# Kernel optimization log

Measured on AMD Instinct MI355X. Metric: run time of the kernel, lower is better.

## Reference

```python
import jax, jax.numpy as jnp
import numpy as np
from jax import lax


def setup_inputs() -> dict:
    key = jax.random.key(0)
    k0, k1, k2, k3 = jax.random.split(key, 4)
    B, Ct, Ht, Wt = 8, 16, 16, 16
    Cm, Hm, Wm = 16, 128, 128
    Cout, K = 64, 3
    template = jax.random.normal(k0, (B, Ct, Ht, Wt), jnp.float32)
    tomatch = jax.random.normal(k1, (B, Cm, Hm, Wm), jnp.float32)
    fan_in = Ct * Cm * K * K
    bound = 1.0 / np.sqrt(fan_in)
    W = jax.random.uniform(k2, (Cout, Ct * Cm, K, K), jnp.float32, -bound, bound)
    b = jax.random.uniform(k3, (Cout,), jnp.float32, -bound, bound)
    return {"template": template, "tomatch": tomatch, "W": W, "b": b}


def _dense_corr(template, tomatch):
    # template: [B, Ct, Ht, Wt], tomatch: [B, Cm, Hm, Wm]
    B, Ct, Ht, Wt = template.shape
    _, Cm, Hm, Wm = tomatch.shape
    # ReplicationPad2d((0, Wt-1, 0, Ht-1)) -> edge pad right/bottom only
    padded = jnp.pad(tomatch, ((0, 0), (0, 0), (0, Ht - 1), (0, Wt - 1)), mode="edge")

    def per_example(tm_pad, tp):
        # tm_pad: [Cm, Hm+Ht-1, Wm+Wt-1] -> treat Cm as batch with 1 channel
        # tp: [Ct, Ht, Wt] -> Ct single-channel filters
        out = lax.conv_general_dilated(
            tm_pad[:, None, :, :],  # [Cm, 1, Hp, Wp] NCHW
            tp[:, None, :, :],      # [Ct, 1, Ht, Wt] OIHW
            window_strides=(1, 1),
            padding="VALID",
        )  # [Cm, Ct, Hm, Wm] (torch conv2d = cross-correlation, same as lax)
        return out.reshape(Cm * Ct, Hm, Wm)  # channel = cm*Ct + ct, matches torch .view

    return jax.vmap(per_example)(padded, template)  # [B, Cm*Ct, Hm, Wm]


def reference(template, tomatch, W, b):
    corr = _dense_corr(template, tomatch)  # [B, Cm*Ct, Hm, Wm]
    out = lax.conv_general_dilated(corr, W, (1, 1), "SAME")  # 3x3 'same' merge conv
    return out + b[None, :, None, None]
```

## Files before the change

kernel.cpp:

```cpp
#include <hip/hip_runtime.h>
#include <hip/hip_bf16.h>


typedef __attribute__((ext_vector_type(4))) float  f32x4;
typedef __attribute__((ext_vector_type(8))) short  bf16x8;

__device__ inline unsigned int pack_bf16x2(float a, float b) {
    unsigned int ua = __builtin_bit_cast(unsigned int, a);
    unsigned int ub = __builtin_bit_cast(unsigned int, b);
    ua = (ua + 0x7fffu + ((ua >> 16) & 1u)) >> 16;
    ub = (ub + 0x7fffu + ((ub >> 16) & 1u)) >> 16;
    return ua | (ub << 16);
}
__device__ inline unsigned short cvt1(float f) {
    unsigned int u = __builtin_bit_cast(unsigned int, f);
    return (unsigned short)((u + 0x7fffu + ((u >> 16) & 1u)) >> 16);
}

__global__ __launch_bounds__(256) void corr_mfma(
    const float* __restrict__ tp, const float* __restrict__ tm,
    unsigned short* __restrict__ corrb)
{
    __shared__ __align__(16) unsigned short smA[2 * 2 * 31 * 82];

    const int t    = threadIdx.x;
    const int wave = t >> 6, lane = t & 63;
    const int n    = lane & 15, quad = lane >> 4;
    const int qh   = quad >> 1, jq = quad & 1;

    const int xh   = (int)blockIdx.x & 1;
    const int y0   = ((int)blockIdx.x >> 1) << 4;
    const int pair = (int)blockIdx.y & 7;
    const int b    = (int)blockIdx.y >> 3;
    const int xg0  = xh << 6;

    for (int cm2 = 0; cm2 < 2; ++cm2) {
        const float* src = tm + (((size_t)(b * 16 + pair * 2 + cm2)) << 14);
        for (int e = t; e < 31 * 80; e += 256) {
            int r = e / 80, c = e - r * 80;
            int gy = y0 + r;  gy = gy > 127 ? 127 : gy;
            int gx = xg0 + c; gx = gx > 127 ? 127 : gx;
            unsigned short h = cvt1(src[(gy << 7) + gx]);
            smA[((cm2 * 2 + 0) * 31 + r) * 82 + c] = h;
            if (c > 0)
                smA[((cm2 * 2 + 1) * 31 + r) * 82 + (c - 1)] = h;
        }
    }
    __syncthreads();

    bf16x8 bq[8];
    {
        const float* tpb = tp + (((size_t)(b * 16 + n)) << 8);
#pragma unroll
        for (int kc = 0; kc < 8; ++kc) {
            const float4* q = (const float4*)(tpb + (((2 * kc + qh) << 4) + (jq << 3)));
            float4 a = q[0], c4 = q[1];
            union { uint4 u; bf16x8 h; } cv;
            cv.u.x = pack_bf16x2(a.x, a.y);
            cv.u.y = pack_bf16x2(a.z, a.w);
            cv.u.z = pack_bf16x2(c4.x, c4.y);
            cv.u.w = pack_bf16x2(c4.z, c4.w);
            bq[kc] = cv.h;
        }
    }

    const unsigned* smAd = (const unsigned*)smA;
    const int PITCH = 41, PLANE = 31 * 41;

#pragma unroll 1
    for (int it = 0; it < 8; ++it) {
        const int lxa  = (wave << 4) + (it << 1);
        const int D00  = (n + qh) * PITCH + ((lxa + (jq << 3)) >> 1);

        f32x4 acc[4];
#pragma unroll
        for (int q = 0; q < 4; ++q) acc[q] = (f32x4){0.f, 0.f, 0.f, 0.f};

#pragma unroll
        for (int kc = 0; kc < 8; ++kc) {
            const int dof = D00 + kc * 82;
#pragma unroll
            for (int ch = 0; ch < 4; ++ch) {
                const int d = dof + ch * PLANE;
                union { uint4 u; bf16x8 h; } fr;
                fr.u.x = smAd[d];     fr.u.y = smAd[d + 1];
                fr.u.z = smAd[d + 2]; fr.u.w = smAd[d + 3];
                const int ai = ((ch & 1) << 1) | (ch >> 1);
                acc[ai] = __builtin_amdgcn_mfma_f32_16x16x32_bf16(
                    bq[kc], fr.h, acc[ai], 0, 0, 0);
            }
        }

        const int y = y0 + n;
#pragma unroll
        for (int ai = 0; ai < 4; ++ai) {
            const int par = ai >> 1, cm2 = ai & 1;
            const int x   = xg0 + lxa + par;
            uint2 v;
            v.x = pack_bf16x2(acc[ai][0], acc[ai][1]);
            v.y = pack_bf16x2(acc[ai][2], acc[ai][3]);
            unsigned short* dst = corrb
                + (((size_t)(b * 16384 + (y << 7) + x)) << 8)
                + (pair << 5) + (cm2 << 4) + (quad << 2);
            *(uint2*)dst = v;
        }
    }
}

__global__ __launch_bounds__(256) void wt_kernel(
    const float* __restrict__ W, unsigned short* __restrict__ Wb)
{
    int idx = (int)blockIdx.x * 256 + (int)threadIdx.x;
    int c  = idx & 255;
    int rem = idx >> 8;
    int co = rem % 64;
    int kk = rem / 64;
    Wb[idx] = cvt1(W[(size_t)co * 2304 + (size_t)c * 9 + kk]);
}

__global__ __launch_bounds__(256) void merge_mfma(
    const unsigned short* __restrict__ corrb, const unsigned short* __restrict__ Wb,
    const float* __restrict__ bias, float* __restrict__ out)
{
    __shared__ __align__(16) unsigned short sm[10 * 34 * 72];

    const int t    = threadIdx.x;
    const int wave = t >> 6, lane = t & 63;
    const int n    = lane & 15, quad = lane >> 4;
    const int x0   = (int)blockIdx.x << 5;
    const int y0   = (int)blockIdx.y << 3;
    const int b    = (int)blockIdx.z;

    f32x4 acc[4][4];
#pragma unroll
    for (int a = 0; a < 4; ++a)
#pragma unroll
        for (int q = 0; q < 4; ++q) acc[a][q] = (f32x4){0.f, 0.f, 0.f, 0.f};

    const unsigned short* cb = corrb + ((size_t)b << 22);

    uint4 v[11];

#define SLAB_LOAD(C0)                                                        \
    {                                                                        \
        _Pragma("unroll")                                                    \
        for (int k = 0; k < 11; ++k) {                                       \
            int e = t + (k << 8);                                            \
            int ci = e & 7, rem = e >> 3;                                    \
            int cc = rem % 34, r = rem / 34;                                 \
            int gy = y0 - 1 + r, gx = x0 - 1 + cc;                           \
            uint4 vv = {0u, 0u, 0u, 0u};                                     \
            if (e < 2720 && (unsigned)gy < 128u && (unsigned)gx < 128u)      \
                vv = *(const uint4*)(cb + (((size_t)((gy << 7) + gx)) << 8)  \
                                        + (C0) + (ci << 3));                 \
            v[k] = vv;                                                       \
        }                                                                    \
    }
#define SLAB_WRITE()                                                         \
    {                                                                        \
        _Pragma("unroll")                                                    \
        for (int k = 0; k < 11; ++k) {                                       \
            int e = t + (k << 8);                                            \
            int ci = e & 7, rem = e >> 3;                                    \
            int cc = rem % 34, r = rem / 34;                                 \
            if (e < 2720)                                                    \
                *(uint4*)&sm[r * 2448 + cc * 72 + (ci << 3)] = v[k];         \
        }                                                                    \
    }

    SLAB_LOAD(0)
    SLAB_WRITE()
    __syncthreads();

#pragma unroll 1
    for (int c0 = 0; c0 < 256; c0 += 64) {
        if (c0 < 192) SLAB_LOAD(c0 + 64)

        const unsigned short* wpb = Wb + (size_t)n * 256 + c0 + (quad << 3);
        bf16x8 afc[4];
        {
#pragma unroll
            for (int ct = 0; ct < 4; ++ct)
                afc[ct] = *(const bf16x8*)(wpb + (size_t)ct * 4096);
        }
#pragma unroll 1
        for (int idx = 0; idx < 18; ++idx) {
            const int nidx = idx < 17 ? idx + 1 : 17;
            const int nkk = nidx >> 1, nkc = nidx & 1;
            bf16x8 afn[4];
#pragma unroll
            for (int ct = 0; ct < 4; ++ct)
                afn[ct] = *(const bf16x8*)(wpb + (size_t)nkk * 16384
                                               + (nkc << 5) + (size_t)ct * 4096);
            const int kk = idx >> 1, kc = idx & 1;
            const int dy = kk / 3, dx = kk - 3 * dy;
#pragma unroll
            for (int nt = 0; nt < 4; ++nt) {
                const int prow = 2 * wave + (nt >> 1) + dy;
                const int pcol = ((nt & 1) << 4) + n + dx;
                bf16x8 bf = *(const bf16x8*)&sm[prow * 2448 + pcol * 72
                                                + (kc << 5) + (quad << 3)];
#pragma unroll
                for (int ct = 0; ct < 4; ++ct)
                    acc[ct][nt] = __builtin_amdgcn_mfma_f32_16x16x32_bf16(
                        afc[ct], bf, acc[ct][nt], 0, 0, 0);
            }
#pragma unroll
            for (int ct = 0; ct < 4; ++ct) afc[ct] = afn[ct];
        }

        __syncthreads();
        if (c0 < 192) SLAB_WRITE()
        __syncthreads();
    }

#pragma unroll
    for (int ct = 0; ct < 4; ++ct) {
#pragma unroll
        for (int nt = 0; nt < 4; ++nt) {
            const int y   = y0 + 2 * wave + (nt >> 1);
            const int x   = x0 + ((nt & 1) << 4) + n;
            const int co0 = (ct << 4) + (quad << 2);
            float* op = out + (((size_t)((b << 6) + co0) << 7) + y) * 128 + x;
#pragma unroll
            for (int r = 0; r < 4; ++r)
                op[(size_t)r << 14] = acc[ct][nt][r] + bias[co0 + r];
        }
    }
#undef SLAB_LOAD
#undef SLAB_WRITE
}

extern "C" void kernel_launch(void* const* d_in, const int* in_sizes, int n_in,
                              void* d_out, int out_size, void* d_ws, size_t ws_size,
                              hipStream_t stream)
{
    const float* tp   = (const float*)d_in[0];
    const float* tm   = (const float*)d_in[1];
    const float* Wt   = (const float*)d_in[2];
    const float* bias = (const float*)d_in[3];
    float* out = (float*)d_out;

    unsigned short* corrb = (unsigned short*)d_ws;
    unsigned short* Wb    = corrb + (size_t)8 * 16384 * 256;

    corr_mfma<<<dim3(16, 64), dim3(256), 0, stream>>>(tp, tm, corrb);
    wt_kernel<<<dim3(576), dim3(256), 0, stream>>>(Wt, Wb);
    merge_mfma<<<dim3(4, 16, 8), dim3(256), 0, stream>>>(corrb, Wb, bias, out);
}
```

Before: 193.6 us.

## Fuse correlation into merge conv, recomputing corr tile with halo in shared memory

Merges the correlation kernel and the 3x3 merge conv into one kernel. Each block computes the bf16 correlation for its 10x34 halo tile directly into shared memory, one group of 4 template-match channels (64 corr channels) per stage, then runs the merge MFMAs on it. This drops the large bf16 corr intermediate in global memory and its write/read traffic. In exchange it recomputes the halo correlation, serializes the corr and merge phases with barriers and no overlap, and moves to 512 threads per block.

```diff
diff --git a/kernel.cpp b/kernel.cpp
--- a/kernel.cpp
+++ b/kernel.cpp
@@ -17,36 +17,33 @@
     return (unsigned short)((u + 0x7fffu + ((u >> 16) & 1u)) >> 16);
 }
 
-__global__ __launch_bounds__(256) void corr_mfma(
+__global__ __launch_bounds__(256) void wt_kernel(
+    const float* __restrict__ W, unsigned short* __restrict__ Wb)
+{
+    int idx = (int)blockIdx.x * 256 + (int)threadIdx.x;
+    int c  = idx & 255;
+    int rem = idx >> 8;
+    int co = rem % 64;
+    int kk = rem / 64;
+    Wb[idx] = cvt1(W[(size_t)co * 2304 + (size_t)c * 9 + kk]);
+}
+
+__global__ __launch_bounds__(512, 4) void fused_mfma(
     const float* __restrict__ tp, const float* __restrict__ tm,
-    unsigned short* __restrict__ corrb)
+    const unsigned short* __restrict__ Wb, const float* __restrict__ bias,
+    float* __restrict__ out)
 {
-    __shared__ __align__(16) unsigned short smA[2 * 2 * 31 * 82];
+    __shared__ __align__(16) unsigned short smC[10 * 34 * 72];
+    __shared__ __align__(16) unsigned short smT[4 * 2 * 25 * 50];
 
     const int t    = threadIdx.x;
     const int wave = t >> 6, lane = t & 63;
     const int n    = lane & 15, quad = lane >> 4;
     const int qh   = quad >> 1, jq = quad & 1;
 
-    const int xh   = (int)blockIdx.x & 1;
-    const int y0   = ((int)blockIdx.x >> 1) << 4;
-    const int pair = (int)blockIdx.y & 7;
-    const int b    = (int)blockIdx.y >> 3;
-    const int xg0  = xh << 6;
-
-    for (int cm2 = 0; cm2 < 2; ++cm2) {
-        const float* src = tm + (((size_t)(b * 16 + pair * 2 + cm2)) << 14);
-        for (int e = t; e < 31 * 80; e += 256) {
-            int r = e / 80, c = e - r * 80;
-            int gy = y0 + r;  gy = gy > 127 ? 127 : gy;
-            int gx = xg0 + c; gx = gx > 127 ? 127 : gx;
-            unsigned short h = cvt1(src[(gy << 7) + gx]);
-            smA[((cm2 * 2 + 0) * 31 + r) * 82 + c] = h;
-            if (c > 0)
-                smA[((cm2 * 2 + 1) * 31 + r) * 82 + (c - 1)] = h;
-        }
-    }
-    __syncthreads();
+    const int x0 = (int)blockIdx.x << 5;
+    const int y0 = (int)blockIdx.y << 3;
+    const int b  = (int)blockIdx.z;
 
     bf16x8 bq[8];
     {
@@ -64,162 +61,108 @@
         }
     }
 
-    const unsigned* smAd = (const unsigned*)smA;
-    const int PITCH = 41, PLANE = 31 * 41;
-
-#pragma unroll 1
-    for (int it = 0; it < 8; ++it) {
-        const int lxa  = (wave << 4) + (it << 1);
-        const int D00  = (n + qh) * PITCH + ((lxa + (jq << 3)) >> 1);
-
-        f32x4 acc[4];
-#pragma unroll
-        for (int q = 0; q < 4; ++q) acc[q] = (f32x4){0.f, 0.f, 0.f, 0.f};
-
-#pragma unroll
-        for (int kc = 0; kc < 8; ++kc) {
-            const int dof = D00 + kc * 82;
-#pragma unroll
-            for (int ch = 0; ch < 4; ++ch) {
-                const int d = dof + ch * PLANE;
-                union { uint4 u; bf16x8 h; } fr;
-                fr.u.x = smAd[d];     fr.u.y = smAd[d + 1];
-                fr.u.z = smAd[d + 2]; fr.u.w = smAd[d + 3];
-                const int ai = ((ch & 1) << 1) | (ch >> 1);
-                acc[ai] = __builtin_amdgcn_mfma_f32_16x16x32_bf16(
-                    bq[kc], fr.h, acc[ai], 0, 0, 0);
-            }
-        }
-
-        const int y = y0 + n;
-#pragma unroll
-        for (int ai = 0; ai < 4; ++ai) {
-            const int par = ai >> 1, cm2 = ai & 1;
-            const int x   = xg0 + lxa + par;
-            uint2 v;
-            v.x = pack_bf16x2(acc[ai][0], acc[ai][1]);
-            v.y = pack_bf16x2(acc[ai][2], acc[ai][3]);
-            unsigned short* dst = corrb
-                + (((size_t)(b * 16384 + (y << 7) + x)) << 8)
-                + (pair << 5) + (cm2 << 4) + (quad << 2);
-            *(uint2*)dst = v;
-        }
-    }
-}
-
-__global__ __launch_bounds__(256) void wt_kernel(
-    const float* __restrict__ W, unsigned short* __restrict__ Wb)
-{
-    int idx = (int)blockIdx.x * 256 + (int)threadIdx.x;
-    int c  = idx & 255;
-    int rem = idx >> 8;
-    int co = rem % 64;
-    int kk = rem / 64;
-    Wb[idx] = cvt1(W[(size_t)co * 2304 + (size_t)c * 9 + kk]);
-}
-
-__global__ __launch_bounds__(256) void merge_mfma(
-    const unsigned short* __restrict__ corrb, const unsigned short* __restrict__ Wb,
-    const float* __restrict__ bias, float* __restrict__ out)
-{
-    __shared__ __align__(16) unsigned short sm[10 * 34 * 72];
-
-    const int t    = threadIdx.x;
-    const int wave = t >> 6, lane = t & 63;
-    const int n    = lane & 15, quad = lane >> 4;
-    const int x0   = (int)blockIdx.x << 5;
-    const int y0   = (int)blockIdx.y << 3;
-    const int b    = (int)blockIdx.z;
-
-    f32x4 acc[4][4];
+    f32x4 acc[4][2];
 #pragma unroll
     for (int a = 0; a < 4; ++a)
 #pragma unroll
-        for (int q = 0; q < 4; ++q) acc[a][q] = (f32x4){0.f, 0.f, 0.f, 0.f};
-
-    const unsigned short* cb = corrb + ((size_t)b << 22);
-
-    uint4 v[11];
-
-#define SLAB_LOAD(C0)                                                        \
-    {                                                                        \
-        _Pragma("unroll")                                                    \
-        for (int k = 0; k < 11; ++k) {                                       \
-            int e = t + (k << 8);                                            \
-            int ci = e & 7, rem = e >> 3;                                    \
-            int cc = rem % 34, r = rem / 34;                                 \
-            int gy = y0 - 1 + r, gx = x0 - 1 + cc;                           \
-            uint4 vv = {0u, 0u, 0u, 0u};                                     \
-            if (e < 2720 && (unsigned)gy < 128u && (unsigned)gx < 128u)      \
-                vv = *(const uint4*)(cb + (((size_t)((gy << 7) + gx)) << 8)  \
-                                        + (C0) + (ci << 3));                 \
-            v[k] = vv;                                                       \
-        }                                                                    \
-    }
-#define SLAB_WRITE()                                                         \
-    {                                                                        \
-        _Pragma("unroll")                                                    \
-        for (int k = 0; k < 11; ++k) {                                       \
-            int e = t + (k << 8);                                            \
-            int ci = e & 7, rem = e >> 3;                                    \
-            int cc = rem % 34, r = rem / 34;                                 \
-            if (e < 2720)                                                    \
-                *(uint4*)&sm[r * 2448 + cc * 72 + (ci << 3)] = v[k];         \
-        }                                                                    \
-    }
-
-    SLAB_LOAD(0)
-    SLAB_WRITE()
-    __syncthreads();
+        for (int q = 0; q < 2; ++q) acc[a][q] = (f32x4){0.f, 0.f, 0.f, 0.f};
 
 #pragma unroll 1
-    for (int c0 = 0; c0 < 256; c0 += 64) {
-        if (c0 < 192) SLAB_LOAD(c0 + 64)
+    for (int s = 0; s < 4; ++s) {
+        {
+            const float* tmb = tm + ((size_t)(b * 16 + (s << 2)) << 14);
+#pragma unroll 1
+            for (int e = t; e < 4900; e += 512) {
+                int cm  = e / 1225;
+                int rem = e - 1225 * cm;
+                int r   = rem / 49;
+                int c   = rem - 49 * r;
+                int gy = y0 - 1 + r; gy = gy < 0 ? 0 : (gy > 127 ? 127 : gy);
+                int gx = x0 - 1 + c; gx = gx < 0 ? 0 : (gx > 127 ? 127 : gx);
+                unsigned short h = cvt1(tmb[((size_t)cm << 14) + (gy << 7) + gx]);
+                smT[((cm * 2 + 0) * 25 + r) * 50 + c] = h;
+                if (c > 0)
+                    smT[((cm * 2 + 1) * 25 + r) * 50 + (c - 1)] = h;
+            }
+        }
+        __syncthreads();
 
-        const unsigned short* wpb = Wb + (size_t)n * 256 + c0 + (quad << 3);
-        bf16x8 afc[4];
         {
+            const unsigned* smTd = (const unsigned*)smT;
+#pragma unroll 1
+            for (int i = 0; i < 11; ++i) {
+                const int g  = wave * 11 + i;
+                const int j  = g / 22;
+                const int tl = g - 22 * j;
+                const int p  = (tl << 4) + n;
+                const int pc = p < 340 ? p : 339;
+                const int py = pc / 34;
+                const int px = pc - 34 * py;
+                const int pl = px & 1;
+                const int base = ((j * 2 + pl) * 25 + py + qh) * 25
+                               + ((px - pl) >> 1) + (jq << 2);
+                f32x4 a4 = (f32x4){0.f, 0.f, 0.f, 0.f};
+#pragma unroll
+                for (int kc = 0; kc < 8; ++kc) {
+                    const int d = base + kc * 50;
+                    union { uint4 u; bf16x8 h; } fr;
+                    fr.u.x = smTd[d];     fr.u.y = smTd[d + 1];
+                    fr.u.z = smTd[d + 2]; fr.u.w = smTd[d + 3];
+                    a4 = __builtin_amdgcn_mfma_f32_16x16x32_bf16(
+                        bq[kc], fr.h, a4, 0, 0, 0);
+                }
+                const int gy = y0 - 1 + py, gx = x0 - 1 + px;
+                const bool valid = ((unsigned)gy < 128u) && ((unsigned)gx < 128u);
+                uint2 v;
+                v.x = valid ? pack_bf16x2(a4[0], a4[1]) : 0u;
+                v.y = valid ? pack_bf16x2(a4[2], a4[3]) : 0u;
+                if (p < 340)
+                    *(uint2*)&smC[p * 72 + (j << 4) + (quad << 2)] = v;
+            }
+        }
+        __syncthreads();
+
+        {
+            const int c0 = s << 6;
+            const unsigned short* wpb = Wb + (size_t)n * 256 + c0 + (quad << 3);
+            bf16x8 afc[4];
 #pragma unroll
             for (int ct = 0; ct < 4; ++ct)
                 afc[ct] = *(const bf16x8*)(wpb + (size_t)ct * 4096);
-        }
 #pragma unroll 1
-        for (int idx = 0; idx < 18; ++idx) {
-            const int nidx = idx < 17 ? idx + 1 : 17;
-            const int nkk = nidx >> 1, nkc = nidx & 1;
-            bf16x8 afn[4];
-#pragma unroll
-            for (int ct = 0; ct < 4; ++ct)
-                afn[ct] = *(const bf16x8*)(wpb + (size_t)nkk * 16384
-                                               + (nkc << 5) + (size_t)ct * 4096);
-            const int kk = idx >> 1, kc = idx & 1;
-            const int dy = kk / 3, dx = kk - 3 * dy;
-#pragma unroll
-            for (int nt = 0; nt < 4; ++nt) {
-                const int prow = 2 * wave + (nt >> 1) + dy;
-                const int pcol = ((nt & 1) << 4) + n + dx;
-                bf16x8 bf = *(const bf16x8*)&sm[prow * 2448 + pcol * 72
-                                                + (kc << 5) + (quad << 3)];
+            for (int idx = 0; idx < 18; ++idx) {
+                const int nidx = idx < 17 ? idx + 1 : 17;
+                const int nkk = nidx >> 1, nkc = nidx & 1;
+                bf16x8 afn[4];
 #pragma unroll
                 for (int ct = 0; ct < 4; ++ct)
-                    acc[ct][nt] = __builtin_amdgcn_mfma_f32_16x16x32_bf16(
-                        afc[ct], bf, acc[ct][nt], 0, 0, 0);
+                    afn[ct] = *(const bf16x8*)(wpb + (size_t)nkk * 16384
+                                                   + (nkc << 5) + (size_t)ct * 4096);
+                const int kk = idx >> 1, kc = idx & 1;
+                const int dy = kk / 3, dx = kk - 3 * dy;
+#pragma unroll
+                for (int nt = 0; nt < 2; ++nt) {
+                    const int prow = wave + dy;
+                    const int pcol = (nt << 4) + n + dx;
+                    bf16x8 bf = *(const bf16x8*)&smC[prow * 2448 + pcol * 72
+                                                     + (kc << 5) + (quad << 3)];
+#pragma unroll
+                    for (int ct = 0; ct < 4; ++ct)
+                        acc[ct][nt] = __builtin_amdgcn_mfma_f32_16x16x32_bf16(
+                            afc[ct], bf, acc[ct][nt], 0, 0, 0);
+                }
+#pragma unroll
+                for (int ct = 0; ct < 4; ++ct) afc[ct] = afn[ct];
             }
-#pragma unroll
-            for (int ct = 0; ct < 4; ++ct) afc[ct] = afn[ct];
         }
-
-        __syncthreads();
-        if (c0 < 192) SLAB_WRITE()
-        __syncthreads();
     }
 
 #pragma unroll
     for (int ct = 0; ct < 4; ++ct) {
 #pragma unroll
-        for (int nt = 0; nt < 4; ++nt) {
-            const int y   = y0 + 2 * wave + (nt >> 1);
-            const int x   = x0 + ((nt & 1) << 4) + n;
+        for (int nt = 0; nt < 2; ++nt) {
+            const int y   = y0 + wave;
+            const int x   = x0 + (nt << 4) + n;
             const int co0 = (ct << 4) + (quad << 2);
             float* op = out + (((size_t)((b << 6) + co0) << 7) + y) * 128 + x;
 #pragma unroll
@@ -227,8 +170,6 @@
                 op[(size_t)r << 14] = acc[ct][nt][r] + bias[co0 + r];
         }
     }
-#undef SLAB_LOAD
-#undef SLAB_WRITE
 }
 
 extern "C" void kernel_launch(void* const* d_in, const int* in_sizes, int n_in,
@@ -241,10 +182,8 @@
     const float* bias = (const float*)d_in[3];
     float* out = (float*)d_out;
 
-    unsigned short* corrb = (unsigned short*)d_ws;
-    unsigned short* Wb    = corrb + (size_t)8 * 16384 * 256;
+    unsigned short* Wb = (unsigned short*)d_ws;
 
-    corr_mfma<<<dim3(16, 64), dim3(256), 0, stream>>>(tp, tm, corrb);
     wt_kernel<<<dim3(576), dim3(256), 0, stream>>>(Wt, Wb);
-    merge_mfma<<<dim3(4, 16, 8), dim3(256), 0, stream>>>(corrb, Wb, bias, out);
+    fused_mfma<<<dim3(4, 16, 8), dim3(512), 0, stream>>>(tp, tm, Wb, bias, out);
 }
```

Result: slower. 250.0 us (+29.2%).
